# Optimization experiments

Measured on AMD Instinct MI355X. Metric: run time of the kernel, lower is better.

## Reference

```python
import jax, jax.numpy as jnp
import numpy as np

N, G, E = 100000, 32768, 1000000
F, H = 64, 64


def _mlp(x, w1, b1, w2, b2):
    # Linear -> SiLU -> Linear (matches nn.Sequential in the torch module)
    return jax.nn.silu(x @ w1 + b1) @ w2 + b2


def setup_inputs() -> dict:
    key = jax.random.key(0)
    ks = jax.random.split(key, 24)

    def lin(k, fan_in, fan_out):
        s = 1.0 / np.sqrt(fan_in)
        kw, kb = jax.random.split(k)
        w = jax.random.uniform(kw, (fan_in, fan_out), jnp.float32, -s, s)
        b = jax.random.uniform(kb, (fan_out,), jnp.float32, -s, s)
        return w, b

    node_w1, node_b1 = lin(ks[0], F, H)
    node_w2, node_b2 = lin(ks[1], H, H)
    edge_w1, edge_b1 = lin(ks[2], 6, H)
    edge_w2, edge_b2 = lin(ks[3], H, H)
    msg_w1, msg_b1 = lin(ks[4], 2 * H, H)
    msg_w2, msg_b2 = lin(ks[5], H, H)
    upd_w1, upd_b1 = lin(ks[6], H, H)
    upd_w2, upd_b2 = lin(ks[7], H, H)

    return {
        "node_features": jax.random.normal(ks[8], (N, F), jnp.float32),
        "node_pos": jax.random.normal(ks[9], (N, 3), jnp.float32),
        "grid_pos": jax.random.normal(ks[10], (G, 3), jnp.float32),
        "orientations": jax.random.normal(ks[11], (N, 3, 3), jnp.float32),
        "edge_index": jnp.stack([
            jax.random.randint(ks[12], (E,), 0, N),
            jax.random.randint(ks[13], (E,), 0, G),
        ]),
        "node_w1": node_w1, "node_b1": node_b1, "node_w2": node_w2, "node_b2": node_b2,
        "edge_w1": edge_w1, "edge_b1": edge_b1, "edge_w2": edge_w2, "edge_b2": edge_b2,
        "msg_w1": msg_w1, "msg_b1": msg_b1, "msg_w2": msg_w2, "msg_b2": msg_b2,
        "upd_w1": upd_w1, "upd_b1": upd_b1, "upd_w2": upd_w2, "upd_b2": upd_b2,
    }


def reference(node_features, node_pos, grid_pos, orientations, edge_index,
              node_w1, node_b1, node_w2, node_b2,
              edge_w1, edge_b1, edge_w2, edge_b2,
              msg_w1, msg_b1, msg_w2, msg_b2,
              upd_w1, upd_b1, upd_w2, upd_b2):
    source, target = edge_index[0], edge_index[1]
    num_grid = grid_pos.shape[0]

    # node MLP
    h_node = _mlp(node_features, node_w1, node_b1, node_w2, node_b2)  # [N,H]

    # per-edge message with orientation-aware projection
    pos_s = node_pos[source]                 # [E,3]
    rel = grid_pos[target] - pos_s           # [E,3]
    # bmm(rel[:,None,:], R[source]).squeeze(1) == einsum ei,eij->ej
    trel = jnp.einsum("ei,eij->ej", rel, orientations[source])
    edge_attr = jnp.concatenate([pos_s, trel], axis=-1)        # [E,6]
    e_feat = _mlp(edge_attr, edge_w1, edge_b1, edge_w2, edge_b2)
    msg_in = jnp.concatenate([h_node[source], e_feat], axis=-1)  # [E,2H]
    messages = _mlp(msg_in, msg_w1, msg_b1, msg_w2, msg_b2)      # [E,H]

    # scatter-mean into grid buckets (mask out-of-range targets)
    valid = (target >= 0) & (target < num_grid)
    idx = jnp.where(valid, target, 0)
    msg_masked = jnp.where(valid[:, None], messages, 0.0)
    sums = jax.ops.segment_sum(msg_masked, idx, num_segments=num_grid)
    cnts = jax.ops.segment_sum(valid.astype(jnp.float32), idx, num_segments=num_grid)
    grid_feat = sums / jnp.maximum(cnts, 1.0)[:, None]

    return _mlp(grid_feat, upd_w1, upd_b1, upd_w2, upd_b2)  # [G,H]
```

## Files before the change

### kernel.cpp

```cpp
#include <hip/hip_runtime.h>
#include <hip/hip_bf16.h>
#include <cstdint>

typedef __attribute__((ext_vector_type(8))) short short8;
typedef __attribute__((ext_vector_type(4))) float f32x4;
typedef unsigned short u16;

__device__ __forceinline__ float b2f(u16 u) {
  union { unsigned int i; float f; } v; v.i = ((unsigned int)u) << 16; return v.f;
}
__device__ __forceinline__ u16 f2b(float f) {
  __hip_bfloat16 h = __float2bfloat16(f);
  union { __hip_bfloat16 h; u16 u; } v; v.h = h; return v.u;
}
__device__ __forceinline__ float silu_f(float x) {
  return x * __builtin_amdgcn_rcpf(1.0f + __expf(-x));
}

__device__ __forceinline__ float loadF(const void* p, long i, int isf32) {
  if (isf32) return ((const float*)p)[i];
  return b2f(((const u16*)p)[i]);
}

__device__ __forceinline__ void gload_lds16(const void* g, void* l) {
  __builtin_amdgcn_global_load_lds(
      (const __attribute__((address_space(1))) void*)g,
      (__attribute__((address_space(3))) void*)l, 16, 0, 0);
}

__device__ __forceinline__ int sniffbit(u16 u) {
  unsigned e = (u >> 7) & 0xffu;
  return (e >= 0xC0u || (e < 0x40u && (u & 0x7fffu) != 0)) ? 1 : 0;
}

struct Ptrs { const void* p[20]; int n[20]; };

#define FW_EW1 0
#define FW_UW1 384
#define FW_UW2 4480
#define FW_UB1 8576
#define FW_UB2 8640
#define FW_EB1 8704
#define FW_EB2 8768
#define FW_MB1 8832
#define FW_MB2 8896
#define FW_TOTAL 8960

#define IMG_EW2 0
#define IMG_MW1 4608
#define IMG_MW2 13312
#define IMG_TOTAL 17920

#define PREP_BLOCKS 105
#define HIST_BLOCKS 1024

__global__ __launch_bounds__(256) void hist_detect_k(
    Ptrs a, const int* __restrict__ eidx, int* __restrict__ cnt8,
    int* __restrict__ flags, long E, int G)
{
  const int t = threadIdx.x;
  const int b = blockIdx.x;
  if (b < HIST_BLOCKS) {
    int* cs = cnt8 + (size_t)(b & 7) * G;
    long i = (long)b * 256 + t;
    const long stride = (long)HIST_BLOCKS * 256;
    for (; i < E; i += stride) {
      int tg = eidx[E + i];
      if (tg >= 0 && tg < G) atomicAdd(&cs[tg], 1);
    }
    return;
  }
  int j = b - HIST_BLOCKS;
  const u16* q = (const u16*)a.p[j];
  int n = a.n[j];
  int m = n < 4096 ? n : 4096;
  int cnt = 0;
  for (int i = t; i < m; i += 256) cnt += sniffbit(q[i]);
  __shared__ int tot;
  if (t == 0) tot = 0;
  __syncthreads();
  if (cnt) atomicAdd(&tot, cnt);
  __syncthreads();
  if (t == 0) flags[j] = (tot >= 2) ? 1 : 0;
}

__global__ __launch_bounds__(256) void scan_prep_node_k(
    Ptrs a, const int* __restrict__ flags,
    const int* __restrict__ cnt8, int* __restrict__ cursor8,
    int* __restrict__ bsum,
    u16* __restrict__ img, float* __restrict__ fw,
    u16* __restrict__ hout, int nrows, int G, int NB2)
{
  const int t = threadIdx.x;
  const int b = blockIdx.x;

  if (b < NB2) {
    __shared__ int sd[256];
    const long tot = 8L * G;
    long j0 = (long)b * 1024 + (long)t * 4;
    int v[4];
#pragma unroll
    for (int k = 0; k < 4; ++k) {
      long j = j0 + k;
      v[k] = (j < tot) ? cnt8[(size_t)(j & 7) * G + (j >> 3)] : 0;
    }
    int local = v[0] + v[1] + v[2] + v[3];
    sd[t] = local;
    __syncthreads();
    for (int off = 1; off < 256; off <<= 1) {
      int x2 = (t >= off) ? sd[t - off] : 0;
      __syncthreads();
      sd[t] += x2;
      __syncthreads();
    }
    int p = sd[t] - local;
#pragma unroll
    for (int k = 0; k < 4; ++k) {
      long j = j0 + k;
      if (j < tot) cursor8[(size_t)(j & 7) * G + (j >> 3)] = p;
      p += v[k];
    }
    if (t == 255) bsum[b] = sd[255];
    return;
  }

  if (b < NB2 + PREP_BLOCKS) {
    int i = (b - NB2) * 256 + t;
    if (i < IMG_TOTAL) {
      const void* bp; int fl; long si; bool real;
      if (i < IMG_MW1) { int nn = i / 72, k = i % 72; bp = a.p[10]; fl = flags[10]; real = k < 64; si = (long)k * 64 + nn; }
      else if (i < IMG_MW2) { int t2 = i - IMG_MW1; int nn = t2 / 136, k = t2 % 136; bp = a.p[12]; fl = flags[12]; real = k < 128; si = (long)k * 64 + nn; }
      else { int t2 = i - IMG_MW2; int nn = t2 / 72, k = t2 % 72; bp = a.p[14]; fl = flags[14]; real = k < 64; si = (long)k * 64 + nn; }
      u16 val = 0;
      if (real) val = f2b(loadF(bp, si, fl));
      img[i] = val;
    } else if (i < IMG_TOTAL + FW_TOTAL) {
      int j = i - IMG_TOTAL;
      const void* bp; int fl; long si;
      if (j < 384)        { bp = a.p[8];  fl = flags[8];  si = j; }
      else if (j < 4480)  { bp = a.p[16]; fl = flags[16]; si = j - 384; }
      else if (j < 8576)  { bp = a.p[18]; fl = flags[18]; si = j - 4480; }
      else {
        int bb = j - 8576; int seg = bb >> 6; si = bb & 63;
        switch (seg) {
          case 0: bp = a.p[17]; fl = flags[17]; break;
          case 1: bp = a.p[19]; fl = flags[19]; break;
          case 2: bp = a.p[9];  fl = flags[9];  break;
          case 3: bp = a.p[11]; fl = flags[11]; break;
          case 4: bp = a.p[13]; fl = flags[13]; break;
          default: bp = a.p[15]; fl = flags[15]; break;
        }
      }
      fw[j] = loadF(bp, si, fl);
    }
    return;
  }

  __shared__ float xs[64][68];
  __shared__ float w1s[64][68];
  __shared__ float w2s[64][68];
  __shared__ float b1s[64];
  __shared__ float b2s[64];
  const void* x = a.p[0];
  const int xf = flags[0], f1 = flags[4], fb1 = flags[5], f2 = flags[6], fb2 = flags[7];
  const long rbase = (long)(b - NB2 - PREP_BLOCKS) * 64;
  for (int i = t; i < 4096; i += 256) {
    int k = i >> 6, cc = i & 63;
    w1s[k][cc] = loadF(a.p[4], i, f1);
    w2s[k][cc] = loadF(a.p[6], i, f2);
  }
  if (t < 64) { b1s[t] = loadF(a.p[5], t, fb1); b2s[t] = loadF(a.p[7], t, fb2); }
  {
    int row = t >> 2, ch = t & 3;
    long rg = rbase + row;
    if (rg < nrows) {
      if (xf) {
        const float* xp = (const float*)x + rg * 64 + ch * 16;
#pragma unroll
        for (int m = 0; m < 16; ++m) xs[row][ch * 16 + m] = xp[m];
      } else {
        const u16* xp = (const u16*)x + rg * 64 + ch * 16;
#pragma unroll
        for (int m = 0; m < 16; ++m) xs[row][ch * 16 + m] = b2f(xp[m]);
      }
    } else {
#pragma unroll
      for (int m = 0; m < 16; ++m) xs[row][ch * 16 + m] = 0.f;
    }
  }
  __syncthreads();
  const int r0 = (t >> 4) * 4, c0 = (t & 15) * 4;
  float acc[4][4];
#pragma unroll
  for (int i = 0; i < 4; ++i)
#pragma unroll
    for (int j = 0; j < 4; ++j) acc[i][j] = b1s[c0 + j];
  for (int k = 0; k < 64; ++k) {
    float w0 = w1s[k][c0], w1v = w1s[k][c0 + 1], w2v = w1s[k][c0 + 2], w3v = w1s[k][c0 + 3];
#pragma unroll
    for (int i = 0; i < 4; ++i) {
      float av = xs[r0 + i][k];
      acc[i][0] = fmaf(av, w0, acc[i][0]);
      acc[i][1] = fmaf(av, w1v, acc[i][1]);
      acc[i][2] = fmaf(av, w2v, acc[i][2]);
      acc[i][3] = fmaf(av, w3v, acc[i][3]);
    }
  }
  __syncthreads();
#pragma unroll
  for (int i = 0; i < 4; ++i)
#pragma unroll
    for (int j = 0; j < 4; ++j) xs[r0 + i][c0 + j] = silu_f(acc[i][j]);
  __syncthreads();
  float acc2[4][4];
#pragma unroll
  for (int i = 0; i < 4; ++i)
#pragma unroll
    for (int j = 0; j < 4; ++j) acc2[i][j] = b2s[c0 + j];
  for (int k = 0; k < 64; ++k) {
    float w0 = w2s[k][c0], w1v = w2s[k][c0 + 1], w2v = w2s[k][c0 + 2], w3v = w2s[k][c0 + 3];
#pragma unroll
    for (int i = 0; i < 4; ++i) {
      float av = xs[r0 + i][k];
      acc2[i][0] = fmaf(av, w0, acc2[i][0]);
      acc2[i][1] = fmaf(av, w1v, acc2[i][1]);
      acc2[i][2] = fmaf(av, w2v, acc2[i][2]);
      acc2[i][3] = fmaf(av, w3v, acc2[i][3]);
    }
  }
#pragma unroll
  for (int i = 0; i < 4; ++i) {
    long rg = rbase + r0 + i;
    if (rg < nrows) {
#pragma unroll
      for (int j = 0; j < 4; ++j) hout[rg * 64 + c0 + j] = f2b(acc2[i][j]);
    }
  }
}

__global__ __launch_bounds__(256) void scat_k(const int* __restrict__ eidx,
                                              int* __restrict__ cursor8,
                                              const int* __restrict__ bsum,
                                              unsigned int* __restrict__ pkS,
                                              int* __restrict__ evp,
                                              long E, int G, int NB2) {
  __shared__ int bo[256];
  const int t = threadIdx.x;
  int v = (t < NB2) ? bsum[t] : 0;
  bo[t] = v;
  __syncthreads();
  for (int off = 1; off < 256; off <<= 1) {
    int x2 = (t >= off) ? bo[t - off] : 0;
    __syncthreads();
    bo[t] += x2;
    __syncthreads();
  }
  if (blockIdx.x == 0 && t == 0) *evp = bo[NB2 - 1];
  int excl = bo[t] - v;
  __syncthreads();
  bo[t] = excl;
  __syncthreads();
  const int c = blockIdx.x & 7;
  int* cur = cursor8 + (size_t)c * G;
  long i = (long)blockIdx.x * 256 + t;
  const long stride = (long)gridDim.x * 256;
  for (; i < E; i += stride) {
    int tg = eidx[E + i];
    if (tg >= 0 && tg < G) {
      int s = eidx[i];
      long j = ((long)tg << 3) | c;
      int p = atomicAdd(&cur[tg], 1) + bo[j >> 10];
      __builtin_nontemporal_store((unsigned int)s | ((unsigned int)tg << 17), pkS + p);
    }
  }
}

#define ETILES 4

__global__ __launch_bounds__(256, 5) void edge_kernel(
    const void* node_pos, const void* grid_pos, const void* orient,
    const unsigned int* __restrict__ pkS, const int* __restrict__ evp,
    const u16* __restrict__ h_node, const u16* __restrict__ img,
    const float* __restrict__ fw, const int* __restrict__ flags,
    float* __restrict__ sums, int G)
{
  __shared__ __align__(16) u16 pool[4][3328];
  __shared__ float eaf[64][6];
  __shared__ float w1e[6][64];
  __shared__ float biasE[4][64];
  __shared__ int tgt_s[64];

  const int t = threadIdx.x;
  const int pf = flags[1], gf = flags[2], of = flags[3];
  const int Ev = *evp;

  const int lane = t & 63, w = t >> 6;
  const int q = lane >> 4, c = lane & 15;
  const int m0 = w * 16;
  u16* hstage = &pool[w][0];
  u16 (* __restrict__ ef1w)[72] = (u16 (*)[72])&pool[w][1024];
  u16 (* __restrict__ efeat)[72] = (u16 (*)[72])&pool[w][2176];
  float (* __restrict__ msgfw)[66] = (float (*)[66])&pool[w][1024];
  const u16* wE2 = img + IMG_EW2;
  const u16* wM1 = img + IMG_MW1;
  const u16* wM2 = img + IMG_MW2;
  const f32x4 z = {0.f, 0.f, 0.f, 0.f};

  const long blockBase = (long)blockIdx.x * (ETILES * 64);

  unsigned int pkA = 0, pkB = 0, pkC = 0, pkD = 0;
  if (lane < 16) {
    long e0 = blockBase + m0 + lane;
    if (e0 < Ev)       pkA = pkS[e0];
    if (e0 + 64 < Ev)  pkB = pkS[e0 + 64];
    if (e0 + 128 < Ev) pkC = pkS[e0 + 128];
    if (e0 + 192 < Ev) pkD = pkS[e0 + 192];
  }

  {
    unsigned int pks = (unsigned int)__shfl((int)pkA, lane & 15);
    int ss = (int)(pks & 0x1FFFFu);
    const u16* gp = h_node + (long)ss * 64 + (size_t)(lane >> 4) * 8;
    gload_lds16(gp, hstage);
    gload_lds16(gp + 32, hstage + 512);
  }

  for (int i = t; i < 384; i += 256) w1e[i / 64][i % 64] = fw[FW_EW1 + i];
  { int seg = t >> 6, cc = t & 63; biasE[seg][cc] = fw[FW_EB1 + seg * 64 + cc]; }
  __syncthreads();

  for (int tile = 0; tile < ETILES; ++tile) {
    long base = blockBase + (long)tile * 64;
    if (base >= Ev) break;

    asm volatile("s_waitcnt vmcnt(0)" ::: "memory");
    __builtin_amdgcn_sched_barrier(0);

    if (lane < 16) {
      long eg = base + m0 + lane;
      int gs = (int)(pkA & 0x1FFFFu);
      int tg = (eg < Ev) ? (int)(pkA >> 17) : -1;
      tgt_s[m0 + lane] = tg;
      int tgc = (tg >= 0) ? tg : 0;
      float ps0 = loadF(node_pos, (long)gs * 3 + 0, pf);
      float ps1 = loadF(node_pos, (long)gs * 3 + 1, pf);
      float ps2 = loadF(node_pos, (long)gs * 3 + 2, pf);
      float rel0 = loadF(grid_pos, (long)tgc * 3 + 0, gf) - ps0;
      float rel1 = loadF(grid_pos, (long)tgc * 3 + 1, gf) - ps1;
      float rel2 = loadF(grid_pos, (long)tgc * 3 + 2, gf) - ps2;
      float o0 = loadF(orient, (long)gs * 9 + 0, of);
      float o1 = loadF(orient, (long)gs * 9 + 1, of);
      float o2 = loadF(orient, (long)gs * 9 + 2, of);
      float o3 = loadF(orient, (long)gs * 9 + 3, of);
      float o4 = loadF(orient, (long)gs * 9 + 4, of);
      float o5 = loadF(orient, (long)gs * 9 + 5, of);
      float o6 = loadF(orient, (long)gs * 9 + 6, of);
      float o7 = loadF(orient, (long)gs * 9 + 7, of);
      float o8 = loadF(orient, (long)gs * 9 + 8, of);
      float tr0 = rel0 * o0; tr0 = fmaf(rel1, o3, tr0); tr0 = fmaf(rel2, o6, tr0);
      float tr1 = rel0 * o1; tr1 = fmaf(rel1, o4, tr1); tr1 = fmaf(rel2, o7, tr1);
      float tr2 = rel0 * o2; tr2 = fmaf(rel1, o5, tr2); tr2 = fmaf(rel2, o8, tr2);
      eaf[m0 + lane][0] = ps0; eaf[m0 + lane][1] = ps1; eaf[m0 + lane][2] = ps2;
      eaf[m0 + lane][3] = tr0; eaf[m0 + lane][4] = tr1; eaf[m0 + lane][5] = tr2;
    }
    __builtin_amdgcn_sched_barrier(0);
    asm volatile("s_waitcnt lgkmcnt(0)" ::: "memory");
    __builtin_amdgcn_s_barrier();
    __builtin_amdgcn_sched_barrier(0);

    {
      int e = lane >> 2, c0 = (lane & 3) * 16;
      int eb = m0 + e;
      float a0 = eaf[eb][0], a1 = eaf[eb][1], a2 = eaf[eb][2];
      float a3 = eaf[eb][3], a4 = eaf[eb][4], a5 = eaf[eb][5];
      __align__(16) u16 tmp[16];
#pragma unroll
      for (int j = 0; j < 16; ++j) {
        int cc = c0 + j;
        float acc = biasE[0][cc];
        acc = fmaf(a0, w1e[0][cc], acc);
        acc = fmaf(a1, w1e[1][cc], acc);
        acc = fmaf(a2, w1e[2][cc], acc);
        acc = fmaf(a3, w1e[3][cc], acc);
        acc = fmaf(a4, w1e[4][cc], acc);
        acc = fmaf(a5, w1e[5][cc], acc);
        tmp[j] = f2b(silu_f(acc));
      }
      *(short8*)&ef1w[e][c0] = *(const short8*)tmp;
      *(short8*)&ef1w[e][c0 + 8] = *(const short8*)(tmp + 8);
    }
    __builtin_amdgcn_wave_barrier();
    {
      short8 a0 = *(const short8*)&ef1w[c][q * 8];
      short8 a1 = *(const short8*)&ef1w[c][32 + q * 8];
#pragma unroll
      for (int nt = 0; nt < 4; ++nt) {
        short8 b0 = *(const short8*)&wE2[(nt * 16 + c) * 72 + q * 8];
        short8 b1v = *(const short8*)&wE2[(nt * 16 + c) * 72 + 32 + q * 8];
        f32x4 acc = __builtin_amdgcn_mfma_f32_16x16x32_bf16(a0, b0, z, 0, 0, 0);
        acc = __builtin_amdgcn_mfma_f32_16x16x32_bf16(a1, b1v, acc, 0, 0, 0);
#pragma unroll
        for (int r = 0; r < 4; ++r) {
          int row = q * 4 + r, col = nt * 16 + c;
          efeat[row][col] = f2b(acc[r] + biasE[1][col]);
        }
      }
    }
    __builtin_amdgcn_wave_barrier();
    {
      short8 a0 = *(const short8*)&hstage[q * 128 + c * 8];
      short8 a1 = *(const short8*)&hstage[512 + q * 128 + c * 8];
      short8 a2 = *(const short8*)&efeat[c][q * 8];
      short8 a3 = *(const short8*)&efeat[c][32 + q * 8];
      __builtin_amdgcn_sched_barrier(0);
      asm volatile("s_waitcnt lgkmcnt(0)" ::: "memory");
      __builtin_amdgcn_sched_barrier(0);
      if (tile + 1 < ETILES && base + 64 < Ev) {
        unsigned int pks = (unsigned int)__shfl((int)pkB, lane & 15);
        int ss = (int)(pks & 0x1FFFFu);
        const u16* gp = h_node + (long)ss * 64 + (size_t)(lane >> 4) * 8;
        gload_lds16(gp, hstage);
        gload_lds16(gp + 32, hstage + 512);
      }
      __builtin_amdgcn_sched_barrier(0);
#pragma unroll
      for (int nt = 0; nt < 4; ++nt) {
        const u16* wp = &wM1[(nt * 16 + c) * 136];
        f32x4 acc = __builtin_amdgcn_mfma_f32_16x16x32_bf16(a0, *(const short8*)(wp + q * 8), z, 0, 0, 0);
        acc = __builtin_amdgcn_mfma_f32_16x16x32_bf16(a1, *(const short8*)(wp + 32 + q * 8), acc, 0, 0, 0);
        acc = __builtin_amdgcn_mfma_f32_16x16x32_bf16(a2, *(const short8*)(wp + 64 + q * 8), acc, 0, 0, 0);
        acc = __builtin_amdgcn_mfma_f32_16x16x32_bf16(a3, *(const short8*)(wp + 96 + q * 8), acc, 0, 0, 0);
#pragma unroll
        for (int r = 0; r < 4; ++r) {
          int row = q * 4 + r, col = nt * 16 + c;
          ef1w[row][col] = f2b(silu_f(acc[r] + biasE[2][col]));
        }
      }
    }
    __builtin_amdgcn_wave_barrier();
    {
      short8 a0 = *(const short8*)&ef1w[c][q * 8];
      short8 a1 = *(const short8*)&ef1w[c][32 + q * 8];
      __builtin_amdgcn_wave_barrier();
#pragma unroll
      for (int nt = 0; nt < 4; ++nt) {
        short8 b0 = *(const short8*)&wM2[(nt * 16 + c) * 72 + q * 8];
        short8 b1v = *(const short8*)&wM2[(nt * 16 + c) * 72 + 32 + q * 8];
        f32x4 acc = __builtin_amdgcn_mfma_f32_16x16x32_bf16(a0, b0, z, 0, 0, 0);
        acc = __builtin_amdgcn_mfma_f32_16x16x32_bf16(a1, b1v, acc, 0, 0, 0);
#pragma unroll
        for (int r = 0; r < 4; ++r) {
          int row = q * 4 + r, col = nt * 16 + c;
          msgfw[row][col] = acc[r] + biasE[3][col];
        }
      }
    }
    __builtin_amdgcn_wave_barrier();

    {
      int col = lane;
      int cur = tgt_s[m0];
      float run = msgfw[0][col];
      bool lopen = (m0 == 0) ? true : (tgt_s[m0 - 1] == cur);
#pragma unroll
      for (int r2 = 1; r2 < 16; ++r2) {
        int tg = tgt_s[m0 + r2];
        float v = msgfw[r2][col];
        if (tg == cur) {
          run += v;
        } else {
          if (cur >= 0) {
            if (lopen) unsafeAtomicAdd(&sums[(long)cur * 64 + col], run);
            else sums[(long)cur * 64 + col] = run;
          }
          cur = tg; run = v; lopen = false;
        }
      }
      bool ropen = (m0 + 16 >= 64) ? true : (tgt_s[m0 + 16] == cur);
      if (cur >= 0) {
        if (lopen || ropen) unsafeAtomicAdd(&sums[(long)cur * 64 + col], run);
        else sums[(long)cur * 64 + col] = run;
      }
    }
    __builtin_amdgcn_sched_barrier(0);
    asm volatile("s_waitcnt lgkmcnt(0)" ::: "memory");
    __builtin_amdgcn_s_barrier();
    __builtin_amdgcn_sched_barrier(0);
    pkA = pkB; pkB = pkC; pkC = pkD;
  }
}

__global__ __launch_bounds__(256) void upd_mlp(
    const float* __restrict__ sums, const int* __restrict__ cnt8,
    const float* __restrict__ fw, float* __restrict__ out, int nrows)
{
  __shared__ float xs[64][68];
  __shared__ float w1s[64][68];
  __shared__ float w2s[64][68];
  __shared__ float b1s[64];
  __shared__ float b2s[64];
  const int t = threadIdx.x;
  const long rbase = (long)blockIdx.x * 64;
  for (int i = t; i < 4096; i += 256) {
    int k = i >> 6, cc = i & 63;
    w1s[k][cc] = fw[FW_UW1 + i];
    w2s[k][cc] = fw[FW_UW2 + i];
  }
  if (t < 64) { b1s[t] = fw[FW_UB1 + t]; b2s[t] = fw[FW_UB2 + t]; }
  {
    int row = t >> 2, ch = t & 3;
    long rg = rbase + row;
    if (rg < nrows) {
      int cn = 0;
#pragma unroll
      for (int cc = 0; cc < 8; ++cc) cn += cnt8[(size_t)cc * nrows + rg];
      float inv = 1.0f / fmaxf((float)cn, 1.0f);
      const float* p = sums + rg * 64 + ch * 16;
#pragma unroll
      for (int m = 0; m < 16; ++m) xs[row][ch * 16 + m] = p[m] * inv;
    } else {
#pragma unroll
      for (int m = 0; m < 16; ++m) xs[row][ch * 16 + m] = 0.f;
    }
  }
  __syncthreads();
  const int r0 = (t >> 4) * 4, c0 = (t & 15) * 4;
  float acc[4][4];
#pragma unroll
  for (int i = 0; i < 4; ++i)
#pragma unroll
    for (int j = 0; j < 4; ++j) acc[i][j] = b1s[c0 + j];
  for (int k = 0; k < 64; ++k) {
    float w0 = w1s[k][c0], w1v = w1s[k][c0 + 1], w2v = w1s[k][c0 + 2], w3v = w1s[k][c0 + 3];
#pragma unroll
    for (int i = 0; i < 4; ++i) {
      float av = xs[r0 + i][k];
      acc[i][0] = fmaf(av, w0, acc[i][0]);
      acc[i][1] = fmaf(av, w1v, acc[i][1]);
      acc[i][2] = fmaf(av, w2v, acc[i][2]);
      acc[i][3] = fmaf(av, w3v, acc[i][3]);
    }
  }
  __syncthreads();
#pragma unroll
  for (int i = 0; i < 4; ++i)
#pragma unroll
    for (int j = 0; j < 4; ++j) xs[r0 + i][c0 + j] = silu_f(acc[i][j]);
  __syncthreads();
  float acc2[4][4];
#pragma unroll
  for (int i = 0; i < 4; ++i)
#pragma unroll
    for (int j = 0; j < 4; ++j) acc2[i][j] = b2s[c0 + j];
  for (int k = 0; k < 64; ++k) {
    float w0 = w2s[k][c0], w1v = w2s[k][c0 + 1], w2v = w2s[k][c0 + 2], w3v = w2s[k][c0 + 3];
#pragma unroll
    for (int i = 0; i < 4; ++i) {
      float av = xs[r0 + i][k];
      acc2[i][0] = fmaf(av, w0, acc2[i][0]);
      acc2[i][1] = fmaf(av, w1v, acc2[i][1]);
      acc2[i][2] = fmaf(av, w2v, acc2[i][2]);
      acc2[i][3] = fmaf(av, w3v, acc2[i][3]);
    }
  }
#pragma unroll
  for (int i = 0; i < 4; ++i) {
    long rg = rbase + r0 + i;
    if (rg < nrows) {
#pragma unroll
      for (int j = 0; j < 4; ++j) out[rg * 64 + c0 + j] = acc2[i][j];
    }
  }
}

extern "C" void kernel_launch(void* const* d_in, const int* in_sizes, int n_in,
                              void* d_out, int out_size, void* d_ws, size_t ws_size,
                              hipStream_t stream) {
  const int N = in_sizes[1] / 3;
  const int G = in_sizes[2] / 3;
  const long E = (long)in_sizes[4] / 2;
  const int NB2 = (int)((8L * G + 1023) / 1024);
  const int nodeBlocks = (N + 63) / 64;

  char* ws = (char*)d_ws;
  float* sums = (float*)ws;
  size_t off = (size_t)G * 256;
  int* cnt8 = (int*)(ws + off);     off += (size_t)G * 32;
  int* cursor8 = (int*)(ws + off);  off += (size_t)G * 32;
  int* bsum = (int*)(ws + off);     off += 1024;
  int* evp = (int*)(ws + off);      off += 256;
  int* flags = (int*)(ws + off);    off += 256;
  unsigned int* pkS = (unsigned int*)(ws + off); off += (size_t)E * 4;
  u16* h_node = (u16*)(ws + off);   off += (size_t)N * 128;
  u16* img = (u16*)(ws + off);      off += (size_t)IMG_TOTAL * 2;
  float* fw = (float*)(ws + off);

  hipMemsetAsync(ws, 0, (size_t)G * 288, stream);

  Ptrs a;
  const int map[20] = {0,1,2,3, 5,6,7,8, 9,10,11,12, 13,14,15,16, 17,18,19,20};
  for (int i = 0; i < 20; ++i) { a.p[i] = d_in[map[i]]; a.n[i] = in_sizes[map[i]]; }

  hist_detect_k<<<HIST_BLOCKS + 20, 256, 0, stream>>>(
      a, (const int*)d_in[4], cnt8, flags, E, G);
  scan_prep_node_k<<<NB2 + PREP_BLOCKS + nodeBlocks, 256, 0, stream>>>(
      a, flags, cnt8, cursor8, bsum, img, fw, h_node, N, G, NB2);
  scat_k<<<1024, 256, 0, stream>>>((const int*)d_in[4], cursor8, bsum, pkS, evp, E, G, NB2);
  edge_kernel<<<(int)((E + ETILES * 64 - 1) / (ETILES * 64)), 256, 0, stream>>>(
      d_in[1], d_in[2], d_in[3], pkS, evp, h_node, img, fw, flags, sums, G);
  upd_mlp<<<(G + 63) / 64, 256, 0, stream>>>(sums, cnt8, fw, (float*)d_out, G);
}
```

Measured before the change: 507.7 us.

## Prefetch next tile's h_node rows and orientations into registers instead of LDS DMA

Replaces the global_load_lds staging of gathered h_node rows with ordinary vector loads into registers, which are written into a combined [16][136] LDS A-operand buffer alongside the edge features. The orientation matrix loads for the next tile are also issued early, overlapping the current tile's atomics epilogue. This removes the explicit vmcnt(0) wait at tile start and simplifies the message-MLP A-operand layout. In exchange it raises register pressure, so launch bounds drop from 5 to 4 waves per SIMD, which may reduce occupancy.

```diff
diff --git a/kernel.cpp b/kernel.cpp
--- a/kernel.cpp
+++ b/kernel.cpp
@@ -20,12 +20,6 @@
 __device__ __forceinline__ float loadF(const void* p, long i, int isf32) {
   if (isf32) return ((const float*)p)[i];
   return b2f(((const u16*)p)[i]);
-}
-
-__device__ __forceinline__ void gload_lds16(const void* g, void* l) {
-  __builtin_amdgcn_global_load_lds(
-      (const __attribute__((address_space(1))) void*)g,
-      (__attribute__((address_space(3))) void*)l, 16, 0, 0);
 }
 
 __device__ __forceinline__ int sniffbit(u16 u) {
@@ -277,7 +271,7 @@
 
 #define ETILES 4
 
-__global__ __launch_bounds__(256, 5) void edge_kernel(
+__global__ __launch_bounds__(256, 4) void edge_kernel(
     const void* node_pos, const void* grid_pos, const void* orient,
     const unsigned int* __restrict__ pkS, const int* __restrict__ evp,
     const u16* __restrict__ h_node, const u16* __restrict__ img,
@@ -297,10 +291,9 @@
   const int lane = t & 63, w = t >> 6;
   const int q = lane >> 4, c = lane & 15;
   const int m0 = w * 16;
-  u16* hstage = &pool[w][0];
-  u16 (* __restrict__ ef1w)[72] = (u16 (*)[72])&pool[w][1024];
-  u16 (* __restrict__ efeat)[72] = (u16 (*)[72])&pool[w][2176];
-  float (* __restrict__ msgfw)[66] = (float (*)[66])&pool[w][1024];
+  u16 (* __restrict__ ef1w)[72] = (u16 (*)[72])&pool[w][0];
+  u16 (* __restrict__ hAw)[136] = (u16 (*)[136])&pool[w][1152];
+  float (* __restrict__ msgfw)[66] = (float (*)[66])&pool[w][1152];
   const u16* wE2 = img + IMG_EW2;
   const u16* wM1 = img + IMG_MW1;
   const u16* wM2 = img + IMG_MW2;
@@ -317,12 +310,27 @@
     if (e0 + 192 < Ev) pkD = pkS[e0 + 192];
   }
 
+  float o0, o1, o2, o3, o4, o5, o6, o7, o8;
+  short8 hv0, hv1;
+
   {
-    unsigned int pks = (unsigned int)__shfl((int)pkA, lane & 15);
+    int gs = (int)(pkA & 0x1FFFFu);
+    if (lane < 16) {
+      o0 = loadF(orient, (long)gs * 9 + 0, of);
+      o1 = loadF(orient, (long)gs * 9 + 1, of);
+      o2 = loadF(orient, (long)gs * 9 + 2, of);
+      o3 = loadF(orient, (long)gs * 9 + 3, of);
+      o4 = loadF(orient, (long)gs * 9 + 4, of);
+      o5 = loadF(orient, (long)gs * 9 + 5, of);
+      o6 = loadF(orient, (long)gs * 9 + 6, of);
+      o7 = loadF(orient, (long)gs * 9 + 7, of);
+      o8 = loadF(orient, (long)gs * 9 + 8, of);
+    }
+    unsigned int pks = (unsigned int)__shfl((int)pkA, lane >> 2);
     int ss = (int)(pks & 0x1FFFFu);
-    const u16* gp = h_node + (long)ss * 64 + (size_t)(lane >> 4) * 8;
-    gload_lds16(gp, hstage);
-    gload_lds16(gp + 32, hstage + 512);
+    const u16* hp = h_node + (long)ss * 64 + (lane & 3) * 16;
+    hv0 = *(const short8*)hp;
+    hv1 = *(const short8*)(hp + 8);
   }
 
   for (int i = t; i < 384; i += 256) w1e[i / 64][i % 64] = fw[FW_EW1 + i];
@@ -332,9 +340,6 @@
   for (int tile = 0; tile < ETILES; ++tile) {
     long base = blockBase + (long)tile * 64;
     if (base >= Ev) break;
-
-    asm volatile("s_waitcnt vmcnt(0)" ::: "memory");
-    __builtin_amdgcn_sched_barrier(0);
 
     if (lane < 16) {
       long eg = base + m0 + lane;
@@ -348,20 +353,16 @@
       float rel0 = loadF(grid_pos, (long)tgc * 3 + 0, gf) - ps0;
       float rel1 = loadF(grid_pos, (long)tgc * 3 + 1, gf) - ps1;
       float rel2 = loadF(grid_pos, (long)tgc * 3 + 2, gf) - ps2;
-      float o0 = loadF(orient, (long)gs * 9 + 0, of);
-      float o1 = loadF(orient, (long)gs * 9 + 1, of);
-      float o2 = loadF(orient, (long)gs * 9 + 2, of);
-      float o3 = loadF(orient, (long)gs * 9 + 3, of);
-      float o4 = loadF(orient, (long)gs * 9 + 4, of);
-      float o5 = loadF(orient, (long)gs * 9 + 5, of);
-      float o6 = loadF(orient, (long)gs * 9 + 6, of);
-      float o7 = loadF(orient, (long)gs * 9 + 7, of);
-      float o8 = loadF(orient, (long)gs * 9 + 8, of);
       float tr0 = rel0 * o0; tr0 = fmaf(rel1, o3, tr0); tr0 = fmaf(rel2, o6, tr0);
       float tr1 = rel0 * o1; tr1 = fmaf(rel1, o4, tr1); tr1 = fmaf(rel2, o7, tr1);
       float tr2 = rel0 * o2; tr2 = fmaf(rel1, o5, tr2); tr2 = fmaf(rel2, o8, tr2);
       eaf[m0 + lane][0] = ps0; eaf[m0 + lane][1] = ps1; eaf[m0 + lane][2] = ps2;
       eaf[m0 + lane][3] = tr0; eaf[m0 + lane][4] = tr1; eaf[m0 + lane][5] = tr2;
+    }
+    {
+      int er = lane >> 2, ch = lane & 3;
+      *(short8*)&hAw[er][ch * 16] = hv0;
+      *(short8*)&hAw[er][ch * 16 + 8] = hv1;
     }
     __builtin_amdgcn_sched_barrier(0);
     asm volatile("s_waitcnt lgkmcnt(0)" ::: "memory");
@@ -402,27 +403,16 @@
 #pragma unroll
         for (int r = 0; r < 4; ++r) {
           int row = q * 4 + r, col = nt * 16 + c;
-          efeat[row][col] = f2b(acc[r] + biasE[1][col]);
+          hAw[row][64 + col] = f2b(acc[r] + biasE[1][col]);
         }
       }
     }
     __builtin_amdgcn_wave_barrier();
     {
-      short8 a0 = *(const short8*)&hstage[q * 128 + c * 8];
-      short8 a1 = *(const short8*)&hstage[512 + q * 128 + c * 8];
-      short8 a2 = *(const short8*)&efeat[c][q * 8];
-      short8 a3 = *(const short8*)&efeat[c][32 + q * 8];
-      __builtin_amdgcn_sched_barrier(0);
-      asm volatile("s_waitcnt lgkmcnt(0)" ::: "memory");
-      __builtin_amdgcn_sched_barrier(0);
-      if (tile + 1 < ETILES && base + 64 < Ev) {
-        unsigned int pks = (unsigned int)__shfl((int)pkB, lane & 15);
-        int ss = (int)(pks & 0x1FFFFu);
-        const u16* gp = h_node + (long)ss * 64 + (size_t)(lane >> 4) * 8;
-        gload_lds16(gp, hstage);
-        gload_lds16(gp + 32, hstage + 512);
-      }
-      __builtin_amdgcn_sched_barrier(0);
+      short8 a0 = *(const short8*)&hAw[c][q * 8];
+      short8 a1 = *(const short8*)&hAw[c][32 + q * 8];
+      short8 a2 = *(const short8*)&hAw[c][64 + q * 8];
+      short8 a3 = *(const short8*)&hAw[c][96 + q * 8];
 #pragma unroll
       for (int nt = 0; nt < 4; ++nt) {
         const u16* wp = &wM1[(nt * 16 + c) * 136];
@@ -456,6 +446,28 @@
       }
     }
     __builtin_amdgcn_wave_barrier();
+
+    __builtin_amdgcn_sched_barrier(0);
+    if (tile + 1 < ETILES && base + 64 < Ev) {
+      int gs2 = (int)(pkB & 0x1FFFFu);
+      if (lane < 16) {
+        o0 = loadF(orient, (long)gs2 * 9 + 0, of);
+        o1 = loadF(orient, (long)gs2 * 9 + 1, of);
+        o2 = loadF(orient, (long)gs2 * 9 + 2, of);
+        o3 = loadF(orient, (long)gs2 * 9 + 3, of);
+        o4 = loadF(orient, (long)gs2 * 9 + 4, of);
+        o5 = loadF(orient, (long)gs2 * 9 + 5, of);
+        o6 = loadF(orient, (long)gs2 * 9 + 6, of);
+        o7 = loadF(orient, (long)gs2 * 9 + 7, of);
+        o8 = loadF(orient, (long)gs2 * 9 + 8, of);
+      }
+      unsigned int pks2 = (unsigned int)__shfl((int)pkB, lane >> 2);
+      int ss2 = (int)(pks2 & 0x1FFFFu);
+      const u16* hp2 = h_node + (long)ss2 * 64 + (lane & 3) * 16;
+      hv0 = *(const short8*)hp2;
+      hv1 = *(const short8*)(hp2 + 8);
+    }
+    __builtin_amdgcn_sched_barrier(0);
 
     {
       int col = lane;
```

New measurement: 481.2 us. 5.2% less time.
